# Performance work log

Hardware: AMD Instinct MI355X
Metric: run time of the kernel (lower is better)

Reference implementation:

```python
import jax, jax.numpy as jnp
import numpy as np

NEG_SLOPE = 0.2  # LeakyReLU slope
PAD = 1          # padding for all 3x3 convs (kernel_size // 2)
K = 9            # 3x3 deformable kernel taps


def _conv2d(x, w, b):
    # x: (B,Cin,H,W), w: (Cout,Cin,3,3) -> (B,Cout,H,W), stride 1, SAME pad
    y = jax.lax.conv_general_dilated(x, w, (1, 1), 'SAME',
                                     dimension_numbers=('NCHW', 'OIHW', 'NCHW'))
    return y + b[None, :, None, None]


def _leaky(x):
    return jnp.where(x >= 0, x, NEG_SLOPE * x)


def _deform_conv(x, offset, w, b):
    # torchvision DeformConv2d, kernel 3x3, stride 1, pad 1, no modulation.
    # x: (B,C,H,W); offset: (B, 2*K, H, W) ordered (dy,dx) per tap; w: (O,C,3,3)
    B, C, H, W = x.shape
    O = w.shape[0]
    off = offset.reshape(B, K, 2, H, W)
    ks = jnp.arange(K)
    ky = (ks // 3).astype(x.dtype)
    kx = (ks % 3).astype(x.dtype)
    iy = jnp.arange(H, dtype=x.dtype)
    ix = jnp.arange(W, dtype=x.dtype)
    # sampling locations: out_pos + tap_pos - pad + learned offset  -> (B,K,H,W)
    py = iy[None, None, :, None] + ky[None, :, None, None] - PAD + off[:, :, 0]
    px = ix[None, None, None, :] + kx[None, :, None, None] - PAD + off[:, :, 1]

    y0 = jnp.floor(py)
    x0 = jnp.floor(px)
    wy = py - y0
    wx = px - x0
    y0i = y0.astype(jnp.int32)
    x0i = x0.astype(jnp.int32)

    def gather(img, yi, xi):  # img: (C,H,W); yi,xi: (K,H,W) -> (C,K,H,W)
        return img[:, yi, xi]
    vgather = jax.vmap(gather)  # over batch

    def corner(yi, xi, wgt):
        valid = (yi >= 0) & (yi < H) & (xi >= 0) & (xi < W)
        yc = jnp.clip(yi, 0, H - 1)
        xc = jnp.clip(xi, 0, W - 1)
        v = vgather(x, yc, xc)  # (B,C,K,H,W)
        return v * (wgt * valid.astype(x.dtype))[:, None]

    val = (corner(y0i, x0i, (1 - wy) * (1 - wx))
           + corner(y0i, x0i + 1, (1 - wy) * wx)
           + corner(y0i + 1, x0i, wy * (1 - wx))
           + corner(y0i + 1, x0i + 1, wy * wx))  # (B,C,K,H,W)
    out = jnp.einsum('bckhw,ock->bohw', val, w.reshape(O, C, K))
    return out + b[None, :, None, None]


def _stage(x, cw, cb, ow, ob, dw, db):
    h = _leaky(_conv2d(x, cw, cb))      # plain conv + LeakyReLU
    off = _conv2d(h, ow, ob)            # offset prediction (18 channels)
    return _leaky(_deform_conv(h, off, dw, db))


def setup_inputs() -> dict:
    key = jax.random.key(0)
    keys = iter(jax.random.split(key, 32))

    def nrm(shape, scale):
        return jax.random.normal(next(keys), shape, jnp.float32) * scale

    inp = {'x': jax.random.normal(next(keys), (4, 64, 128, 128), jnp.float32)}
    specs = [(64, 128), (128, 128), (128, 64)]
    for i, (ci, co) in enumerate(specs, 1):
        inp[f's{i}_cw'] = nrm((co, ci, 3, 3), (ci * 9) ** -0.5)
        inp[f's{i}_cb'] = jnp.zeros((co,), jnp.float32)
        inp[f's{i}_ow'] = nrm((18, co, 3, 3), 0.1 * (co * 9) ** -0.5)  # small offsets
        inp[f's{i}_ob'] = jnp.zeros((18,), jnp.float32)
        inp[f's{i}_dw'] = nrm((co, co, 3, 3), (co * 9) ** -0.5)
        inp[f's{i}_db'] = jnp.zeros((co,), jnp.float32)
    return inp


def reference(x,
              s1_cw, s1_cb, s1_ow, s1_ob, s1_dw, s1_db,
              s2_cw, s2_cb, s2_ow, s2_ob, s2_dw, s2_db,
              s3_cw, s3_cb, s3_ow, s3_ob, s3_dw, s3_db):
    x = _stage(x, s1_cw, s1_cb, s1_ow, s1_ob, s1_dw, s1_db)
    x = _stage(x, s2_cw, s2_cb, s2_ow, s2_ob, s2_dw, s2_db)
    x = _stage(x, s3_cw, s3_cb, s3_ow, s3_ob, s3_dw, s3_db)
    return x
```

## Files before the change

### kernel.cpp

```cpp
#include <hip/hip_runtime.h>
#include <hip/hip_bf16.h>

#define HW 128
#define HW2 16384
#define NEG 0.2f

typedef __attribute__((ext_vector_type(8))) short short8;
typedef __attribute__((ext_vector_type(4))) float f32x4;
typedef __attribute__((ext_vector_type(2))) float f32x2;

__device__ __forceinline__ float lrelu(float v) { return v >= 0.f ? v : NEG * v; }
__device__ __forceinline__ unsigned short f2bf(float f) {
    unsigned int u = __float_as_uint(f);
    u = (u + 0x7fffu + ((u >> 16) & 1u)) >> 16;
    return (unsigned short)u;
}
__device__ __forceinline__ unsigned int pk2(float a, float b) {
    __hip_bfloat162 h = __float22bfloat162_rn(float2{a, b});
    return *(unsigned int*)&h;
}
__device__ __forceinline__ float2 upk(unsigned int u) {
    return float2{__uint_as_float(u << 16), __uint_as_float(u & 0xffff0000u)};
}
__device__ __forceinline__ f32x2 upkv(unsigned int u) {
    f32x2 r;
    r.x = __uint_as_float(u << 16);
    r.y = __uint_as_float(u & 0xffff0000u);
    return r;
}

struct WSeg { const float* s; unsigned short* d; int K9; int NMT; int validM; int n; };
struct WArgs { WSeg seg[9]; };

__global__ void wrepack_kernel(WArgs a)
{
    const WSeg sg = a.seg[blockIdx.y];
    int i = blockIdx.x * 256 + threadIdx.x;
    if (i >= sg.n) return;
    int cl = i & 7, lane = (i >> 3) & 63;
    int rest = i >> 9;
    int mt = rest % sg.NMT, gs = rest / sg.NMT;
    int st = gs % 3, g = gs / 3;
    int quad = lane >> 4, l15 = lane & 15;
    int co = mt * 16 + l15, tap = st * 4 + quad;
    unsigned short v = 0;
    if (tap < 9 && co < sg.validM)
        v = f2bf(sg.s[(size_t)co * sg.K9 + (g * 8 + cl) * 9 + tap]);
    sg.d[i] = v;
}

template <int MTW, int SRCF>
__global__ __launch_bounds__(256, 4) void fused_conv(
    const void* __restrict__ actv, const unsigned short* __restrict__ wpad,
    const float* __restrict__ bias, unsigned short* __restrict__ outb,
    float* __restrict__ outf, int Cin, int Cout, int mode)
{
    constexpr int PB = 136 * 16;
    constexpr int SMB = 64 * 136 * 2;
    __shared__ char smem[SMB];
    unsigned short* Es = (unsigned short*)smem;

    const int t = threadIdx.x;
    const int tile = blockIdx.x, b = blockIdx.z;
    const int lane = t & 63, wv = t >> 6, quad = lane >> 4, l15 = lane & 15;
    const int y0 = (tile >> 2) * 2, x0 = (tile & 3) * 32;
    const int ngrp = Cin >> 3;
    const int NSTR = (Cout >> 4) * 512;

    const bool sok = lane < 34;
    const int gy = y0 - 1 + wv, gx = x0 - 1 + lane;
    const bool pok = sok && gy >= 0 && gy < HW && gx >= 0 && gx < HW;
    const int gp = pok ? gy * HW + gx : 0;
    const int slot = wv * 34 + lane;

    const float* actf = (const float*)actv;
    const unsigned short* acth = (const unsigned short*)actv;
    const size_t bofs = (size_t)b * Cin * HW2;

    int baddr[3][4];
#pragma unroll
    for (int st = 0; st < 3; ++st) {
        int tap = st * 4 + quad; tap = tap > 8 ? 8 : tap;
        int ky = (tap * 11) >> 5, kx = tap - 3 * ky;
#pragma unroll
        for (int nt = 0; nt < 4; ++nt) {
            int p = nt * 16 + l15, ly = p >> 5, lx = p & 31;
            baddr[st][nt] = ((ly + ky) * 34 + lx + kx) * 16;
        }
    }
    size_t abase[MTW];
#pragma unroll
    for (int m = 0; m < MTW; ++m)
        abase[m] = (size_t)((wv * MTW + m) * 512 + lane * 8);

    f32x4 acc[MTW][4];
#pragma unroll
    for (int m = 0; m < MTW; ++m)
#pragma unroll
        for (int nt = 0; nt < 4; ++nt) acc[m][nt] = (f32x4)(0.f);

    auto load_grp = [&](int g) -> uint4 {
        uint4 u; u.x = u.y = u.z = u.w = 0;
        if (!pok) return u;
        if (SRCF == 1) {
            u = *(const uint4*)(acth + bofs + ((size_t)g * HW2 + gp) * 8);
        } else {
            const float* pl = actf + bofs + (size_t)(g * 8) * HW2 + gp;
            float v0 = pl[0], v1 = pl[HW2], v2 = pl[2 * HW2], v3 = pl[3 * HW2];
            float v4 = pl[4 * HW2], v5 = pl[5 * HW2], v6 = pl[6 * HW2], v7 = pl[7 * HW2];
            u.x = pk2(v0, v1); u.y = pk2(v2, v3);
            u.z = pk2(v4, v5); u.w = pk2(v6, v7);
        }
        return u;
    };

    short8 apre[MTW][3];
    auto loadA = [&](int g) {
#pragma unroll
        for (int st = 0; st < 3; ++st)
#pragma unroll
            for (int m = 0; m < MTW; ++m)
                apre[m][st] = *(const short8*)(wpad + (size_t)(g * 3 + st) * NSTR + abase[m]);
    };

    uint4 cur = load_grp(0);
    if (sok) *(uint4*)(smem + slot * 16) = cur;
    loadA(0);
    if (ngrp > 1) cur = load_grp(1);
    __syncthreads();

    for (int g = 0; g < ngrp; ++g) {
        char* pb = smem + (g & 1) * PB;
#pragma unroll
        for (int st = 0; st < 3; ++st) {
            short8 bfr[4];
#pragma unroll
            for (int nt = 0; nt < 4; ++nt)
                bfr[nt] = *(const short8*)(pb + baddr[st][nt]);
#pragma unroll
            for (int m = 0; m < MTW; ++m) {
                short8 a = apre[m][st];
#pragma unroll
                for (int nt = 0; nt < 4; ++nt)
                    acc[m][nt] = __builtin_amdgcn_mfma_f32_16x16x32_bf16(
                        a, bfr[nt], acc[m][nt], 0, 0, 0);
            }
        }
        if (g + 1 < ngrp) {
            if (sok) *(uint4*)(smem + ((g + 1) & 1) * PB + slot * 16) = cur;
            loadA(g + 1);
            if (g + 2 < ngrp) cur = load_grp(g + 2);
        }
        __syncthreads();
    }

    if (mode == 0) {
        constexpr int ESTR = 136;
#pragma unroll
        for (int m = 0; m < MTW; ++m) {
            int cb = (wv * MTW + m) * 16;
#pragma unroll
            for (int nt = 0; nt < 4; ++nt) {
                int px = nt * 16 + l15;
                int co = cb + quad * 4;
                unsigned int u0 = pk2(lrelu(acc[m][nt][0] + bias[co]),
                                      lrelu(acc[m][nt][1] + bias[co + 1]));
                unsigned int u1 = pk2(lrelu(acc[m][nt][2] + bias[co + 2]),
                                      lrelu(acc[m][nt][3] + bias[co + 3]));
                uint2 u; u.x = u0; u.y = u1;
                *(uint2*)&Es[px * ESTR + co] = u;
            }
        }
        __syncthreads();
        const int ng8 = Cout >> 3;
        unsigned short* ob = outb + (size_t)b * Cout * HW2;
        for (int tt = t; tt < 64 * ng8; tt += 256) {
            int cg = tt >> 6, px = tt & 63;
            int gp2 = (y0 + (px >> 5)) * HW + x0 + (px & 31);
            *(uint4*)(ob + ((size_t)cg * HW2 + gp2) * 8) =
                *(const uint4*)&Es[px * ESTR + cg * 8];
        }
    } else {
        float* of = outf + (size_t)b * 18 * HW2;
#pragma unroll
        for (int m = 0; m < MTW; ++m) {
            int cb = (wv * MTW + m) * 16;
#pragma unroll
            for (int nt = 0; nt < 4; ++nt) {
                int px = nt * 16 + l15;
                int gp2 = (y0 + (px >> 5)) * HW + x0 + (px & 31);
#pragma unroll
                for (int r = 0; r < 4; ++r) {
                    int co = cb + quad * 4 + r;
                    if (co < 18)
                        of[(size_t)co * HW2 + gp2] = acc[m][nt][r] + bias[co];
                }
            }
        }
    }
}

template <int MTW>
__global__ __launch_bounds__(256, 4) void fused_deform(
    const unsigned short* __restrict__ acth,
    const unsigned short* __restrict__ woff, const float* __restrict__ obias,
    const unsigned short* __restrict__ wpad, const float* __restrict__ bias,
    unsigned short* __restrict__ outb, float* __restrict__ outf,
    int Cin, int Cout, int mode)
{
    constexpr int PATW = 43, PATR = 8, PATP = PATR * PATW;
    constexpr int CSTR = 104;
    constexpr int PB = PATP * 16;
    constexpr int CB = 64 * CSTR * 2;
    constexpr int SMB = 2 * PB + 2 * CB;
    constexpr int OPB = 136 * 16;
    __shared__ char smem[SMB];
    unsigned short* Es = (unsigned short*)smem;

    const int t = threadIdx.x;
    const int tile = blockIdx.x, b = blockIdx.z;
    const int lane = t & 63, wv = t >> 6, quad = lane >> 4, l15 = lane & 15;
    const int y0 = (tile >> 2) * 2, x0 = (tile & 3) * 32;
    const int ngrp = Cin >> 3;
    const int NSTR = (Cout >> 4) * 512;
    const int py0 = y0 - 3, px0 = x0 - 5;
    const size_t bofs = (size_t)b * Cin * HW2;

    for (int i = t; i < 384; i += 256) {
        int bu = i / 192;
        int ii = i - 192 * bu;
        int p = ii / 3, j = ii - 3 * p;
        uint4 z; z.x = z.y = z.z = z.w = 0;
        *(uint4*)(smem + 2 * PB + bu * CB + (p * CSTR + 72 + j * 8) * 2) = z;
    }

    {
        float* offbuf = (float*)(smem + 2 * OPB);
        const bool asok = lane < 34;
        const int agy = y0 - 1 + wv, agx = x0 - 1 + lane;
        const bool apok = asok && agy >= 0 && agy < HW && agx >= 0 && agx < HW;
        const int agp = apok ? agy * HW + agx : 0;
        const int aslot = wv * 34 + lane;

        const int mtile = wv & 1, npair = wv >> 1;
        int obad[3][2];
#pragma unroll
        for (int st = 0; st < 3; ++st) {
            int tap = st * 4 + quad; tap = tap > 8 ? 8 : tap;
            int ky = (tap * 11) >> 5, kx = tap - 3 * ky;
#pragma unroll
            for (int nn = 0; nn < 2; ++nn) {
                int p = (2 * npair + nn) * 16 + l15, ly = p >> 5, lx = p & 31;
                obad[st][nn] = ((ly + ky) * 34 + lx + kx) * 16;
            }
        }
        const size_t oa0 = (size_t)(mtile * 512 + lane * 8);

        f32x4 oacc[2];
        oacc[0] = (f32x4)(0.f); oacc[1] = (f32x4)(0.f);
        short8 oapre[3];
        auto loadAO = [&](int g) {
#pragma unroll
            for (int st = 0; st < 3; ++st)
                oapre[st] = *(const short8*)(woff + (size_t)(g * 3 + st) * 1024 + oa0);
        };
        auto load_g = [&](int g) -> uint4 {
            uint4 u; u.x = u.y = u.z = u.w = 0;
            if (apok) u = *(const uint4*)(acth + bofs + ((size_t)g * HW2 + agp) * 8);
            return u;
        };

        uint4 cur = load_g(0);
        if (asok) *(uint4*)(smem + aslot * 16) = cur;
        loadAO(0);
        if (ngrp > 1) cur = load_g(1);
        __syncthreads();

        for (int g = 0; g < ngrp; ++g) {
            const char* pb = smem + (g & 1) * OPB;
#pragma unroll
            for (int st = 0; st < 3; ++st) {
                short8 a = oapre[st];
#pragma unroll
                for (int nn = 0; nn < 2; ++nn) {
                    short8 bf = *(const short8*)(pb + obad[st][nn]);
                    oacc[nn] = __builtin_amdgcn_mfma_f32_16x16x32_bf16(
                        a, bf, oacc[nn], 0, 0, 0);
                }
            }
            if (g + 1 < ngrp) {
                if (asok) *(uint4*)(smem + ((g + 1) & 1) * OPB + aslot * 16) = cur;
                loadAO(g + 1);
                if (g + 2 < ngrp) cur = load_g(g + 2);
            }
            __syncthreads();
        }

        {
            int co0 = mtile * 16 + quad * 4;
            if (co0 < 18) {
#pragma unroll
                for (int nn = 0; nn < 2; ++nn) {
                    int px = (2 * npair + nn) * 16 + l15;
#pragma unroll
                    for (int r = 0; r < 4; ++r)
                        if (co0 + r < 18)
                            offbuf[px * 20 + co0 + r] = oacc[nn][r] + obias[co0 + r];
                }
            }
        }
        __syncthreads();
    }
    const float* offbuf = (const float*)(smem + 2 * OPB);

    float w00[3], w01[3], w10[3], w11[3];
    int pbase[3], csad[3], svalid[3];
    int allin = 1;
    {
#pragma unroll
        for (int s = 0; s < 3; ++s) {
            int task = t + s * 256;
            svalid[s] = task < 576;
            int task2 = svalid[s] ? task : 0;
            int p = task2 / 9, k = task2 - 9 * p;
            int yy = y0 + (p >> 5), xx = x0 + (p & 31);
            float2 dd = *(const float2*)(offbuf + p * 20 + 2 * k);
            float dy = dd.x, dx = dd.y;
            float py = (float)(yy + k / 3 - 1) + dy;
            float px = (float)(xx + k % 3 - 1) + dx;
            float fy = floorf(py), fx = floorf(px);
            float wy = py - fy, wx = px - fx;
            int iy = (int)fy, ix = (int)fx;
            w00[s] = (1.f - wy) * (1.f - wx);
            w01[s] = (1.f - wy) * wx;
            w10[s] = wy * (1.f - wx);
            w11[s] = wy * wx;
            pbase[s] = ((iy - py0) * PATW + (ix - px0)) * 16;
            csad[s] = (p * CSTR + k * 8) * 2;
            bool ip = iy >= py0 && iy + 1 <= py0 + (PATR - 1)
                   && ix >= px0 && ix + 1 <= px0 + (PATW - 1);
            if (!ip) allin = 0;
        }
    }
    const int fast = __syncthreads_and(allin);

    const int s0 = wv * 86 + lane;
    const int r0 = s0 / PATW, c0_ = s0 - PATW * r0;
    const int gy0_ = py0 + r0, gx0_ = px0 + c0_;
    const bool ok0 = gy0_ >= 0 && gy0_ < HW && gx0_ >= 0 && gx0_ < HW;
    const int go0 = ok0 ? gy0_ * HW + gx0_ : 0;
    const bool has1 = lane < 22;
    const int s1 = wv * 86 + 64 + lane;
    const int r1 = s1 / PATW, c1_ = s1 - PATW * r1;
    const int gy1_ = py0 + r1, gx1_ = px0 + c1_;
    const bool ok1 = has1 && gy1_ >= 0 && gy1_ < HW && gx1_ >= 0 && gx1_ < HW;
    const int go1 = ok1 ? gy1_ * HW + gx1_ : 0;

    size_t abase[MTW];
#pragma unroll
    for (int m = 0; m < MTW; ++m)
        abase[m] = (size_t)((wv * MTW + m) * 512 + lane * 8);
    const int bb0 = l15 * (CSTR * 2) + quad * 16;

    f32x4 acc[MTW][4];
#pragma unroll
    for (int m = 0; m < MTW; ++m)
#pragma unroll
        for (int nt = 0; nt < 4; ++nt) acc[m][nt] = (f32x4)(0.f);

    short8 apre[MTW][3];
    auto loadA = [&](int g) {
#pragma unroll
        for (int st = 0; st < 3; ++st)
#pragma unroll
            for (int m = 0; m < MTW; ++m)
                apre[m][st] = *(const short8*)(wpad + (size_t)(g * 3 + st) * NSTR + abase[m]);
    };

    auto mfma_pre = [&](const char* cs) {
#pragma unroll
        for (int st = 0; st < 3; ++st) {
            short8 bfr[4];
#pragma unroll
            for (int nt = 0; nt < 4; ++nt)
                bfr[nt] = *(const short8*)(cs + bb0 + nt * 16 * (CSTR * 2) + st * 64);
#pragma unroll
            for (int m = 0; m < MTW; ++m) {
                short8 a = apre[m][st];
#pragma unroll
                for (int nt = 0; nt < 4; ++nt)
                    acc[m][nt] = __builtin_amdgcn_mfma_f32_16x16x32_bf16(
                        a, bfr[nt], acc[m][nt], 0, 0, 0);
            }
        }
    };

    if (fast) {
        uint4 u0, u1;
        u0.x = u0.y = u0.z = u0.w = 0; u1 = u0;
        if (ok0) u0 = *(const uint4*)(acth + bofs + (size_t)go0 * 8);
        if (ok1) u1 = *(const uint4*)(acth + bofs + (size_t)go1 * 8);
        *(uint4*)(smem + s0 * 16) = u0;
        if (has1) *(uint4*)(smem + s1 * 16) = u1;
        if (ngrp > 1) {
            u0.x = u0.y = u0.z = u0.w = 0; u1 = u0;
            if (ok0) u0 = *(const uint4*)(acth + bofs + ((size_t)HW2 + go0) * 8);
            if (ok1) u1 = *(const uint4*)(acth + bofs + ((size_t)HW2 + go1) * 8);
        }
        __syncthreads();

        for (int g = 0; g < ngrp; ++g) {
            const char* pb = smem + (g & 1) * PB;
            char* csW = smem + 2 * PB + (g & 1) * CB;

            if (g > 0)
                mfma_pre(smem + 2 * PB + ((g - 1) & 1) * CB);

#pragma unroll
            for (int s = 0; s < 3; ++s) {
                if (!svalid[s]) continue;
                const char* base = pb + pbase[s];
                uint4 c00 = *(const uint4*)base;
                uint4 c01 = *(const uint4*)(base + 16);
                uint4 c10 = *(const uint4*)(base + PATW * 16);
                uint4 c11 = *(const uint4*)(base + PATW * 16 + 16);
                f32x2 vw0 = (f32x2)(w00[s]), vw1 = (f32x2)(w01[s]);
                f32x2 vw2 = (f32x2)(w10[s]), vw3 = (f32x2)(w11[s]);
                f32x2 a0 = vw0 * upkv(c00.x) + vw1 * upkv(c01.x)
                         + vw2 * upkv(c10.x) + vw3 * upkv(c11.x);
                f32x2 a1 = vw0 * upkv(c00.y) + vw1 * upkv(c01.y)
                         + vw2 * upkv(c10.y) + vw3 * upkv(c11.y);
                f32x2 a2 = vw0 * upkv(c00.z) + vw1 * upkv(c01.z)
                         + vw2 * upkv(c10.z) + vw3 * upkv(c11.z);
                f32x2 a3 = vw0 * upkv(c00.w) + vw1 * upkv(c01.w)
                         + vw2 * upkv(c10.w) + vw3 * upkv(c11.w);
                uint4 ou;
                ou.x = pk2(a0.x, a0.y); ou.y = pk2(a1.x, a1.y);
                ou.z = pk2(a2.x, a2.y); ou.w = pk2(a3.x, a3.y);
                *(uint4*)(csW + csad[s]) = ou;
            }

            if (g + 1 < ngrp) {
                char* pn = smem + ((g + 1) & 1) * PB;
                *(uint4*)(pn + s0 * 16) = u0;
                if (has1) *(uint4*)(pn + s1 * 16) = u1;
            }
            loadA(g);
            if (g + 2 < ngrp) {
                u0.x = u0.y = u0.z = u0.w = 0; u1 = u0;
                if (ok0) u0 = *(const uint4*)(acth + bofs +
                                              ((size_t)(g + 2) * HW2 + go0) * 8);
                if (ok1) u1 = *(const uint4*)(acth + bofs +
                                              ((size_t)(g + 2) * HW2 + go1) * 8);
            }
            __syncthreads();
        }
        mfma_pre(smem + 2 * PB + ((ngrp - 1) & 1) * CB);
    } else {
        char* csW = smem + 2 * PB;
        for (int g = 0; g < ngrp; ++g) {
            const unsigned short* gb = acth + bofs + (size_t)g * HW2 * 8;
#pragma unroll
            for (int s = 0; s < 3; ++s) {
                if (!svalid[s]) continue;
                int task = t + s * 256;
                int p = task / 9, k = task - 9 * p;
                int yy = y0 + (p >> 5), xx = x0 + (p & 31);
                float2 dd = *(const float2*)(offbuf + p * 20 + 2 * k);
                float dy = dd.x, dx = dd.y;
                float py = (float)(yy + k / 3 - 1) + dy;
                float px = (float)(xx + k % 3 - 1) + dx;
                float fy = floorf(py), fx = floorf(px);
                float wy = py - fy, wx = px - fx;
                int iy = (int)fy, ix = (int)fx;
                float f0 = 0, f1 = 0, f2 = 0, f3 = 0, f4 = 0, f5 = 0, f6 = 0, f7 = 0;
#pragma unroll
                for (int q = 0; q < 4; ++q) {
                    int ddy = q >> 1, ddx = q & 1;
                    int sy = iy + ddy, sx = ix + ddx;
                    float w = (ddy ? wy : 1.f - wy) * (ddx ? wx : 1.f - wx);
                    if (sy < 0 || sy >= HW || sx < 0 || sx >= HW) w = 0.f;
                    int cy = min(max(sy, 0), HW - 1), cx = min(max(sx, 0), HW - 1);
                    uint4 c = *(const uint4*)(gb + (size_t)(cy * HW + cx) * 8);
                    float2 p0 = upk(c.x), p1 = upk(c.y), p2 = upk(c.z), p3 = upk(c.w);
                    f0 += w * p0.x; f1 += w * p0.y; f2 += w * p1.x; f3 += w * p1.y;
                    f4 += w * p2.x; f5 += w * p2.y; f6 += w * p3.x; f7 += w * p3.y;
                }
                uint4 ou;
                ou.x = pk2(f0, f1); ou.y = pk2(f2, f3);
                ou.z = pk2(f4, f5); ou.w = pk2(f6, f7);
                *(uint4*)(csW + csad[s]) = ou;
            }
            __syncthreads();
            loadA(g);
            mfma_pre(csW);
            __syncthreads();
        }
    }

    __syncthreads();
    if (mode == 0) {
        constexpr int ESTR = 136;
#pragma unroll
        for (int m = 0; m < MTW; ++m) {
            int cb = (wv * MTW + m) * 16;
#pragma unroll
            for (int nt = 0; nt < 4; ++nt) {
                int px = nt * 16 + l15;
                int co = cb + quad * 4;
                unsigned int u0 = pk2(lrelu(acc[m][nt][0] + bias[co]),
                                      lrelu(acc[m][nt][1] + bias[co + 1]));
                unsigned int u1 = pk2(lrelu(acc[m][nt][2] + bias[co + 2]),
                                      lrelu(acc[m][nt][3] + bias[co + 3]));
                uint2 u; u.x = u0; u.y = u1;
                *(uint2*)&Es[px * ESTR + co] = u;
            }
        }
        __syncthreads();
        const int ng8 = Cout >> 3;
        unsigned short* ob = outb + (size_t)b * Cout * HW2;
        for (int tt = t; tt < 64 * ng8; tt += 256) {
            int cg = tt >> 6, px = tt & 63;
            int gp2 = (y0 + (px >> 5)) * HW + x0 + (px & 31);
            *(uint4*)(ob + ((size_t)cg * HW2 + gp2) * 8) =
                *(const uint4*)&Es[px * ESTR + cg * 8];
        }
    } else {
        float* of = outf + (size_t)b * Cout * HW2;
#pragma unroll
        for (int m = 0; m < MTW; ++m) {
            int cb = (wv * MTW + m) * 16;
#pragma unroll
            for (int nt = 0; nt < 4; ++nt) {
                int px = nt * 16 + l15;
                int gp2 = (y0 + (px >> 5)) * HW + x0 + (px & 31);
#pragma unroll
                for (int r = 0; r < 4; ++r) {
                    int co = cb + quad * 4 + r;
                    of[(size_t)co * HW2 + gp2] = lrelu(acc[m][nt][r] + bias[co]);
                }
            }
        }
    }
}

extern "C" void kernel_launch(void* const* d_in, const int* in_sizes, int n_in,
                              void* d_out, int out_size, void* d_ws,
                              size_t ws_size, hipStream_t stream)
{
    const float* x = (const float*)d_in[0];
    const float* p[18];
    for (int i = 0; i < 18; ++i) p[i] = (const float*)d_in[1 + i];

    char* ws = (char*)d_ws;
    unsigned short* A1 = (unsigned short*)ws;
    unsigned short* A2 = (unsigned short*)(ws + 16777216);
    unsigned short* WB = (unsigned short*)(ws + 38273024);

    unsigned short* Wc1 = WB;
    unsigned short* Wo1 = Wc1 + 98304;
    unsigned short* Wd1 = Wo1 + 98304;
    unsigned short* Wc2 = Wd1 + 196608;
    unsigned short* Wo2 = Wc2 + 196608;
    unsigned short* Wd2 = Wo2 + 98304;
    unsigned short* Wc3 = Wd2 + 196608;
    unsigned short* Wo3 = Wc3 + 98304;
    unsigned short* Wd3 = Wo3 + 49152;

    WArgs wa;
    wa.seg[0] = {p[0],  Wc1,  576, 8, 128,  98304};
    wa.seg[1] = {p[2],  Wo1, 1152, 2,  18,  49152};
    wa.seg[2] = {p[4],  Wd1, 1152, 8, 128, 196608};
    wa.seg[3] = {p[6],  Wc2, 1152, 8, 128, 196608};
    wa.seg[4] = {p[8],  Wo2, 1152, 2,  18,  49152};
    wa.seg[5] = {p[10], Wd2, 1152, 8, 128, 196608};
    wa.seg[6] = {p[12], Wc3, 1152, 4,  64,  98304};
    wa.seg[7] = {p[14], Wo3,  576, 2,  18,  24576};
    wa.seg[8] = {p[16], Wd3,  576, 4,  64,  49152};
    wrepack_kernel<<<dim3(768, 9), 256, 0, stream>>>(wa);

    dim3 g(256, 1, 4);
    fused_conv<2, 0><<<g, 256, 0, stream>>>(x, Wc1, p[1], A1, nullptr, 64, 128, 0);
    fused_deform<2><<<g, 256, 0, stream>>>(A1, Wo1, p[3], Wd1, p[5], A2, nullptr, 128, 128, 0);
    fused_conv<2, 1><<<g, 256, 0, stream>>>(A2, Wc2, p[7], A1, nullptr, 128, 128, 0);
    fused_deform<2><<<g, 256, 0, stream>>>(A1, Wo2, p[9], Wd2, p[11], A2, nullptr, 128, 128, 0);
    fused_conv<1, 1><<<g, 256, 0, stream>>>(A2, Wc3, p[13], A1, nullptr, 128, 64, 0);
    fused_deform<1><<<g, 256, 0, stream>>>(A1, Wo3, p[15], Wd3, p[17], nullptr, (float*)d_out, 64, 64, 1);
}
```

Measured before the change: 300.3 us.

## Switch deformable conv GEMM to 32x32x16 MFMA with 2-tap K packing

The deform conv's main GEMM moves from 16x16x32 bf16 MFMA to 32x32x16 bf16 MFMA. Each K step now packs two taps across the lane halves, so 9 taps fit in 5 K-steps instead of 3x4 slots. That removes the padded 12th-tap waste and shrinks the column buffer stride. Weights are repacked into a new layout, and waves split into 2 M-halves by 2 pixel halves, which changes the epilogue mapping. The intent is fewer wasted MACs and fewer LDS B-fragment loads per MFMA, in exchange for larger accumulator register tiles and a redone weight layout.

After: 290.9 us. -3.1%, faster.

```diff
diff --git a/kernel.cpp b/kernel.cpp
--- a/kernel.cpp
+++ b/kernel.cpp
@@ -8,6 +8,7 @@
 typedef __attribute__((ext_vector_type(8))) short short8;
 typedef __attribute__((ext_vector_type(4))) float f32x4;
 typedef __attribute__((ext_vector_type(2))) float f32x2;
+typedef __attribute__((ext_vector_type(16))) float f32x16;
 
 __device__ __forceinline__ float lrelu(float v) { return v >= 0.f ? v : NEG * v; }
 __device__ __forceinline__ unsigned short f2bf(float f) {
@@ -29,7 +30,7 @@
     return r;
 }
 
-struct WSeg { const float* s; unsigned short* d; int K9; int NMT; int validM; int n; };
+struct WSeg { const float* s; unsigned short* d; int K9; int NMT; int validM; int n; int mode; };
 struct WArgs { WSeg seg[9]; };
 
 __global__ void wrepack_kernel(WArgs a)
@@ -39,13 +40,22 @@
     if (i >= sg.n) return;
     int cl = i & 7, lane = (i >> 3) & 63;
     int rest = i >> 9;
-    int mt = rest % sg.NMT, gs = rest / sg.NMT;
-    int st = gs % 3, g = gs / 3;
-    int quad = lane >> 4, l15 = lane & 15;
-    int co = mt * 16 + l15, tap = st * 4 + quad;
     unsigned short v = 0;
-    if (tap < 9 && co < sg.validM)
-        v = f2bf(sg.s[(size_t)co * sg.K9 + (g * 8 + cl) * 9 + tap]);
+    if (sg.mode == 0) {
+        int mt = rest % sg.NMT, gs = rest / sg.NMT;
+        int st = gs % 3, g = gs / 3;
+        int quad = lane >> 4, l15 = lane & 15;
+        int co = mt * 16 + l15, tap = st * 4 + quad;
+        if (tap < 9 && co < sg.validM)
+            v = f2bf(sg.s[(size_t)co * sg.K9 + (g * 8 + cl) * 9 + tap]);
+    } else {
+        int mt = rest % sg.NMT, kig = rest / sg.NMT;
+        int ki = kig % 5, g = kig / 5;
+        int hi = lane >> 5, l31 = lane & 31;
+        int co = mt * 32 + l31, tap = ki * 2 + hi;
+        if (tap < 9 && co < sg.validM)
+            v = f2bf(sg.s[(size_t)co * sg.K9 + (g * 8 + cl) * 9 + tap]);
+    }
     sg.d[i] = v;
 }
 
@@ -209,7 +219,7 @@
     int Cin, int Cout, int mode)
 {
     constexpr int PATW = 43, PATR = 8, PATP = PATR * PATW;
-    constexpr int CSTR = 104;
+    constexpr int CSTR = 88;
     constexpr int PB = PATP * 16;
     constexpr int CB = 64 * CSTR * 2;
     constexpr int SMB = 2 * PB + 2 * CB;
@@ -220,18 +230,17 @@
     const int t = threadIdx.x;
     const int tile = blockIdx.x, b = blockIdx.z;
     const int lane = t & 63, wv = t >> 6, quad = lane >> 4, l15 = lane & 15;
+    const int l31 = lane & 31, hi = lane >> 5;
     const int y0 = (tile >> 2) * 2, x0 = (tile & 3) * 32;
     const int ngrp = Cin >> 3;
-    const int NSTR = (Cout >> 4) * 512;
+    const int NSTR2 = MTW * 1024;
     const int py0 = y0 - 3, px0 = x0 - 5;
     const size_t bofs = (size_t)b * Cin * HW2;
 
-    for (int i = t; i < 384; i += 256) {
-        int bu = i / 192;
-        int ii = i - 192 * bu;
-        int p = ii / 3, j = ii - 3 * p;
+    for (int i = t; i < 128; i += 256) {
+        int bu = i >> 6, p = i & 63;
         uint4 z; z.x = z.y = z.z = z.w = 0;
-        *(uint4*)(smem + 2 * PB + bu * CB + (p * CSTR + 72 + j * 8) * 2) = z;
+        *(uint4*)(smem + 2 * PB + bu * CB + (p * CSTR + 72) * 2) = z;
     }
 
     {
@@ -356,42 +365,34 @@
     const bool ok1 = has1 && gy1_ >= 0 && gy1_ < HW && gx1_ >= 0 && gx1_ < HW;
     const int go1 = ok1 ? gy1_ * HW + gx1_ : 0;
 
-    size_t abase[MTW];
-#pragma unroll
-    for (int m = 0; m < MTW; ++m)
-        abase[m] = (size_t)((wv * MTW + m) * 512 + lane * 8);
-    const int bb0 = l15 * (CSTR * 2) + quad * 16;
-
-    f32x4 acc[MTW][4];
-#pragma unroll
-    for (int m = 0; m < MTW; ++m)
-#pragma unroll
-        for (int nt = 0; nt < 4; ++nt) acc[m][nt] = (f32x4)(0.f);
-
-    short8 apre[MTW][3];
+    size_t abase2[MTW];
+#pragma unroll
+    for (int tt = 0; tt < MTW; ++tt)
+        abase2[tt] = (size_t)(((wv >> 1) * MTW + tt) * 512 + lane * 8);
+    const int bb2 = ((wv & 1) * 32 + l31) * (CSTR * 2) + hi * 16;
+
+    f32x16 acc2[MTW];
+#pragma unroll
+    for (int tt = 0; tt < MTW; ++tt) acc2[tt] = (f32x16)(0.f);
+
+    short8 apre[MTW][5];
     auto loadA = [&](int g) {
 #pragma unroll
-        for (int st = 0; st < 3; ++st)
-#pragma unroll
-            for (int m = 0; m < MTW; ++m)
-                apre[m][st] = *(const short8*)(wpad + (size_t)(g * 3 + st) * NSTR + abase[m]);
+        for (int ki = 0; ki < 5; ++ki)
+#pragma unroll
+            for (int tt = 0; tt < MTW; ++tt)
+                apre[tt][ki] = *(const short8*)(
+                    wpad + (size_t)(g * 5 + ki) * NSTR2 + abase2[tt]);
     };
 
-    auto mfma_pre = [&](const char* cs) {
-#pragma unroll
-        for (int st = 0; st < 3; ++st) {
-            short8 bfr[4];
-#pragma unroll
-            for (int nt = 0; nt < 4; ++nt)
-                bfr[nt] = *(const short8*)(cs + bb0 + nt * 16 * (CSTR * 2) + st * 64);
-#pragma unroll
-            for (int m = 0; m < MTW; ++m) {
-                short8 a = apre[m][st];
-#pragma unroll
-                for (int nt = 0; nt < 4; ++nt)
-                    acc[m][nt] = __builtin_amdgcn_mfma_f32_16x16x32_bf16(
-                        a, bfr[nt], acc[m][nt], 0, 0, 0);
-            }
+    auto mfma32 = [&](const char* cs) {
+#pragma unroll
+        for (int ki = 0; ki < 5; ++ki) {
+            short8 bf = *(const short8*)(cs + bb2 + ki * 32);
+#pragma unroll
+            for (int tt = 0; tt < MTW; ++tt)
+                acc2[tt] = __builtin_amdgcn_mfma_f32_32x32x16_bf16(
+                    apre[tt][ki], bf, acc2[tt], 0, 0, 0);
         }
     };
 
@@ -414,7 +415,7 @@
             char* csW = smem + 2 * PB + (g & 1) * CB;
 
             if (g > 0)
-                mfma_pre(smem + 2 * PB + ((g - 1) & 1) * CB);
+                mfma32(smem + 2 * PB + ((g - 1) & 1) * CB);
 
 #pragma unroll
             for (int s = 0; s < 3; ++s) {
@@ -455,7 +456,7 @@
             }
             __syncthreads();
         }
-        mfma_pre(smem + 2 * PB + ((ngrp - 1) & 1) * CB);
+        mfma32(smem + 2 * PB + ((ngrp - 1) & 1) * CB);
     } else {
         char* csW = smem + 2 * PB;
         for (int g = 0; g < ngrp; ++g) {
@@ -493,27 +494,27 @@
             }
             __syncthreads();
             loadA(g);
-            mfma_pre(csW);
+            mfma32(csW);
             __syncthreads();
         }
     }
 
     __syncthreads();
+    const int px2 = (wv & 1) * 32 + l31;
     if (mode == 0) {
         constexpr int ESTR = 136;
 #pragma unroll
-        for (int m = 0; m < MTW; ++m) {
-            int cb = (wv * MTW + m) * 16;
-#pragma unroll
-            for (int nt = 0; nt < 4; ++nt) {
-                int px = nt * 16 + l15;
-                int co = cb + quad * 4;
-                unsigned int u0 = pk2(lrelu(acc[m][nt][0] + bias[co]),
-                                      lrelu(acc[m][nt][1] + bias[co + 1]));
-                unsigned int u1 = pk2(lrelu(acc[m][nt][2] + bias[co + 2]),
-                                      lrelu(acc[m][nt][3] + bias[co + 3]));
+        for (int tt = 0; tt < MTW; ++tt) {
+            int mtb = ((wv >> 1) * MTW + tt) * 32;
+#pragma unroll
+            for (int q = 0; q < 4; ++q) {
+                int co = mtb + q * 8 + hi * 4;
+                unsigned int u0 = pk2(lrelu(acc2[tt][q * 4 + 0] + bias[co]),
+                                      lrelu(acc2[tt][q * 4 + 1] + bias[co + 1]));
+                unsigned int u1 = pk2(lrelu(acc2[tt][q * 4 + 2] + bias[co + 2]),
+                                      lrelu(acc2[tt][q * 4 + 3] + bias[co + 3]));
                 uint2 u; u.x = u0; u.y = u1;
-                *(uint2*)&Es[px * ESTR + co] = u;
+                *(uint2*)&Es[px2 * ESTR + co] = u;
             }
         }
         __syncthreads();
@@ -527,18 +528,17 @@
         }
     } else {
         float* of = outf + (size_t)b * Cout * HW2;
-#pragma unroll
-        for (int m = 0; m < MTW; ++m) {
-            int cb = (wv * MTW + m) * 16;
-#pragma unroll
-            for (int nt = 0; nt < 4; ++nt) {
-                int px = nt * 16 + l15;
-                int gp2 = (y0 + (px >> 5)) * HW + x0 + (px & 31);
-#pragma unroll
-                for (int r = 0; r < 4; ++r) {
-                    int co = cb + quad * 4 + r;
-                    of[(size_t)co * HW2 + gp2] = lrelu(acc[m][nt][r] + bias[co]);
-                }
+        int gp2 = (y0 + (px2 >> 5)) * HW + x0 + (px2 & 31);
+#pragma unroll
+        for (int tt = 0; tt < MTW; ++tt) {
+            int mtb = ((wv >> 1) * MTW + tt) * 32;
+#pragma unroll
+            for (int q = 0; q < 4; ++q) {
+                int co = mtb + q * 8 + hi * 4;
+#pragma unroll
+                for (int rr = 0; rr < 4; ++rr)
+                    of[(size_t)(co + rr) * HW2 + gp2] =
+                        lrelu(acc2[tt][q * 4 + rr] + bias[co + rr]);
             }
         }
     }
@@ -559,24 +559,24 @@
 
     unsigned short* Wc1 = WB;
     unsigned short* Wo1 = Wc1 + 98304;
-    unsigned short* Wd1 = Wo1 + 98304;
-    unsigned short* Wc2 = Wd1 + 196608;
+    unsigned short* Wd1 = Wo1 + 49152;
+    unsigned short* Wc2 = Wd1 + 163840;
     unsigned short* Wo2 = Wc2 + 196608;
-    unsigned short* Wd2 = Wo2 + 98304;
-    unsigned short* Wc3 = Wd2 + 196608;
+    unsigned short* Wd2 = Wo2 + 49152;
+    unsigned short* Wc3 = Wd2 + 163840;
     unsigned short* Wo3 = Wc3 + 98304;
-    unsigned short* Wd3 = Wo3 + 49152;
+    unsigned short* Wd3 = Wo3 + 24576;
 
     WArgs wa;
-    wa.seg[0] = {p[0],  Wc1,  576, 8, 128,  98304};
-    wa.seg[1] = {p[2],  Wo1, 1152, 2,  18,  49152};
-    wa.seg[2] = {p[4],  Wd1, 1152, 8, 128, 196608};
-    wa.seg[3] = {p[6],  Wc2, 1152, 8, 128, 196608};
-    wa.seg[4] = {p[8],  Wo2, 1152, 2,  18,  49152};
-    wa.seg[5] = {p[10], Wd2, 1152, 8, 128, 196608};
-    wa.seg[6] = {p[12], Wc3, 1152, 4,  64,  98304};
-    wa.seg[7] = {p[14], Wo3,  576, 2,  18,  24576};
-    wa.seg[8] = {p[16], Wd3,  576, 4,  64,  49152};
+    wa.seg[0] = {p[0],  Wc1,  576, 8, 128,  98304, 0};
+    wa.seg[1] = {p[2],  Wo1, 1152, 2,  18,  49152, 0};
+    wa.seg[2] = {p[4],  Wd1, 1152, 4, 128, 163840, 1};
+    wa.seg[3] = {p[6],  Wc2, 1152, 8, 128, 196608, 0};
+    wa.seg[4] = {p[8],  Wo2, 1152, 2,  18,  49152, 0};
+    wa.seg[5] = {p[10], Wd2, 1152, 4, 128, 163840, 1};
+    wa.seg[6] = {p[12], Wc3, 1152, 4,  64,  98304, 0};
+    wa.seg[7] = {p[14], Wo3,  576, 2,  18,  24576, 0};
+    wa.seg[8] = {p[16], Wd3,  576, 2,  64,  40960, 1};
     wrepack_kernel<<<dim3(768, 9), 256, 0, stream>>>(wa);
 
     dim3 g(256, 1, 4);
```
